# Optimization experiments

Measured on AMD Instinct MI355X. Metric: run time of the kernel, lower is better.

Reference implementation:

```python
import jax, jax.numpy as jnp
import numpy as np

EPS = 1e-5

def _layernorm(x, g, b):
    mu = jnp.mean(x, axis=-1, keepdims=True)
    var = jnp.mean(jnp.square(x - mu), axis=-1, keepdims=True)
    return (x - mu) * jax.lax.rsqrt(var + EPS) * g + b

def _knn_gather(x, idx):
    # x: (B, M, C), idx: (B, N, K) -> (B, N, K, C)
    return jax.vmap(lambda m, i: m[i])(x, idx)

def setup_inputs() -> dict:
    key = jax.random.key(0)
    B, N, M, K, C = 1, 8192, 8192, 32, 256
    ks = jax.random.split(key, 24)
    w = lambda k, *s: (jax.random.normal(k, s, dtype=jnp.float32) * 0.02)
    inp = {
        "input_states": jax.random.normal(ks[0], (B, N, C), dtype=jnp.float32),
        "memory_states": jax.random.normal(ks[1], (B, M, C), dtype=jnp.float32),
        "indices": jax.random.randint(ks[2], (B, N, K), 0, M, dtype=jnp.int32),
        "input_coord": jax.random.normal(ks[3], (B, N, 3), dtype=jnp.float32),
        "memory_coord": jax.random.normal(ks[4], (B, M, 3), dtype=jnp.float32),
        "attention_mask": jnp.ones((B, N, K), dtype=jnp.float32),
        "Wq": w(ks[5], C, C), "bq": jnp.zeros((C,), jnp.float32),
        "Wk": w(ks[6], C, C), "bk": jnp.zeros((C,), jnp.float32),
        "Wv": w(ks[7], C, C), "bv": jnp.zeros((C,), jnp.float32),
        "Wo": w(ks[8], C, C), "bo": jnp.zeros((C,), jnp.float32),
        "ln1_g": jnp.ones((C,), jnp.float32), "ln1_b": jnp.zeros((C,), jnp.float32),
        "Wrpe": w(ks[9], C // 2, 3), "brpe": jnp.zeros((C // 2,), jnp.float32),
        "We": w(ks[10], 2 * C, C), "be": jnp.zeros((2 * C,), jnp.float32),
        "Ws": w(ks[11], C, 2 * C), "bs": jnp.zeros((C,), jnp.float32),
        "ln2_g": jnp.ones((C,), jnp.float32), "ln2_b": jnp.zeros((C,), jnp.float32),
    }
    return inp

def reference(input_states, memory_states, indices, input_coord, memory_coord,
              attention_mask, Wq, bq, Wk, bk, Wv, bv, Wo, bo, ln1_g, ln1_b,
              Wrpe, brpe, We, be, Ws, bs, ln2_g, ln2_b):
    B, N, C = input_states.shape
    H = 8
    Ch = C // H
    q = input_states @ Wq.T + bq                                   # (B,N,C)
    k = _knn_gather(memory_states @ Wk.T + bk, indices)            # (B,N,K,C)
    v = _knn_gather(memory_states @ Wv.T + bv, indices)            # (B,N,K,C)
    # rotary positional encoding on relative coordinates
    rel = _knn_gather(memory_coord, indices) - input_coord[:, :, None, :]  # (B,N,K,3)
    ang = rel @ Wrpe.T + brpe                                      # (B,N,K,C/2)
    cos, sin = jnp.cos(ang), jnp.sin(ang)
    k2 = k.reshape(*k.shape[:-1], C // 2, 2)
    x0, x1 = k2[..., 0], k2[..., 1]
    k = jnp.stack([x0 * cos - x1 * sin, x0 * sin + x1 * cos], axis=-1).reshape(k.shape)
    # multi-head attention over K gathered neighbors
    qh = q.reshape(B, N, H, Ch)
    kh = k.reshape(B, N, -1, H, Ch)
    vh = v.reshape(B, N, -1, H, Ch)
    scores = jnp.einsum('bnhc,bnkhc->bhnk', qh, kh) / np.sqrt(Ch).astype(np.float32)
    scores = scores - 1e6 * (1.0 - attention_mask[:, None, :, :])
    attn = jax.nn.softmax(scores, axis=-1)
    hidden = jnp.einsum('bhnk,bnkhc->bnhc', attn, vh).reshape(B, N, C)
    hidden = hidden @ Wo.T + bo
    out = _layernorm(hidden + input_states, ln1_g, ln1_b)
    ff = jax.nn.relu(out @ We.T + be) @ Ws.T + bs
    return _layernorm(out + ff, ln2_g, ln2_b)
```

## Files before the change

kernel.cpp:

```cpp
#include <hip/hip_runtime.h>
#include <hip/hip_bf16.h>
#include <stdint.h>

typedef __attribute__((ext_vector_type(8))) __bf16 bf16x8;
typedef __attribute__((ext_vector_type(8))) unsigned short u16x8;
typedef __attribute__((ext_vector_type(4))) float f32x4;

__device__ inline float bf2f(unsigned short u) {
  union { unsigned u; float f; } z; z.u = ((unsigned)u) << 16; return z.f;
}
__device__ inline unsigned short f2bf(float f) {
  union { float f; unsigned u; } z; z.f = f;
  unsigned r = z.u + 0x7fffu + ((z.u >> 16) & 1u);
  return (unsigned short)(r >> 16);
}
__device__ inline void gload_lds16(const void* g, void* l) {
  __builtin_amdgcn_global_load_lds((const __attribute__((address_space(1))) void*)g,
                                   (__attribute__((address_space(3))) void*)l, 16, 0, 0);
}

__global__ __launch_bounds__(256, 2) void gemm_proj(
    const float* __restrict__ x, const float* __restrict__ mem,
    const float* __restrict__ Wq, const float* __restrict__ Wk, const float* __restrict__ Wv,
    const float* __restrict__ Wo, const float* __restrict__ We, const float* __restrict__ Ws,
    const float* __restrict__ Wrpe, const float* __restrict__ brpe,
    const float* __restrict__ bq, const float* __restrict__ bk, const float* __restrict__ bv,
    unsigned short* __restrict__ qbuf, unsigned short* __restrict__ kbp,
    unsigned short* __restrict__ vbp,
    unsigned short* __restrict__ wob, unsigned short* __restrict__ web,
    unsigned short* __restrict__ wsb, float4* __restrict__ rpe4) {
  const int tid = threadIdx.x;
  const int by = blockIdx.y;
  const long bm = blockIdx.x;

  if (by == 6) {
#pragma unroll
    for (int it = 0; it < 3; ++it) {
      const int j = (int)bm + 128 * it;
      if (j < 64) {
        const float4 v = *(const float4*)(Wo + (long)j * 1024 + tid * 4);
        ushort4 o; o.x = f2bf(v.x); o.y = f2bf(v.y); o.z = f2bf(v.z); o.w = f2bf(v.w);
        *(ushort4*)(wob + (long)j * 1024 + tid * 4) = o;
      } else if (j < 192) {
        const float4 v = *(const float4*)(We + (long)(j - 64) * 1024 + tid * 4);
        ushort4 o; o.x = f2bf(v.x); o.y = f2bf(v.y); o.z = f2bf(v.z); o.w = f2bf(v.w);
        *(ushort4*)(web + (long)(j - 64) * 1024 + tid * 4) = o;
      } else if (j < 320) {
        const float4 v = *(const float4*)(Ws + (long)(j - 192) * 1024 + tid * 4);
        ushort4 o; o.x = f2bf(v.x); o.y = f2bf(v.y); o.z = f2bf(v.z); o.w = f2bf(v.w);
        *(ushort4*)(wsb + (long)(j - 192) * 1024 + tid * 4) = o;
      } else if (j == 320) {
        if (tid < 128) {
          float4 r;
          r.x = Wrpe[3 * tid]; r.y = Wrpe[3 * tid + 1]; r.z = Wrpe[3 * tid + 2]; r.w = brpe[tid];
          rpe4[tid] = r;
        }
      }
    }
    return;
  }

  __shared__ __attribute__((aligned(16))) char lds[4096 + 8192];
  const int lane = tid & 63;
  const int wm = tid >> 7, wo = (tid >> 6) & 1;

  const float* Ab; const float* Wf; const float* biasp; unsigned short* outp; int cb;
  if (by < 2)      { Ab = x;   Wf = Wq + (long)by * 128 * 256;       biasp = bq + by * 128;       outp = qbuf; cb = by * 128; }
  else if (by < 4) { Ab = mem; Wf = Wk + (long)(by - 2) * 128 * 256; biasp = bk + (by - 2) * 128; outp = kbp;  cb = (by - 2) * 128; }
  else             { Ab = mem; Wf = Wv + (long)(by - 4) * 128 * 256; biasp = bv + (by - 4) * 128; outp = vbp;  cb = (by - 4) * 128; }

  f32x4 acc[2][4] = {};
  for (int kt = 0; kt < 8; ++kt) {
#pragma unroll
    for (int c = 0; c < 2; ++c) {
      const int fb = c * 4096 + tid * 16;
      const int row = fb >> 7, colb = fb & 127;
      const float4 a4 = *(const float4*)((const char*)Ab + (bm * 64 + row) * 1024 + kt * 128 + colb);
      ushort4 o; o.x = f2bf(a4.x); o.y = f2bf(a4.y); o.z = f2bf(a4.z); o.w = f2bf(a4.w);
      *(ushort4*)(lds + row * 64 + (colb >> 1)) = o;
    }
#pragma unroll
    for (int c = 0; c < 4; ++c) {
      const int fb = c * 4096 + tid * 16;
      const int row = fb >> 7, colb = fb & 127;
      const float4 a4 = *(const float4*)((const char*)Wf + (long)row * 1024 + kt * 128 + colb);
      ushort4 o; o.x = f2bf(a4.x); o.y = f2bf(a4.y); o.z = f2bf(a4.z); o.w = f2bf(a4.w);
      *(ushort4*)(lds + 4096 + row * 64 + (colb >> 1)) = o;
    }
    __syncthreads();
    bf16x8 af[2], bfr[4];
    const int kb = (lane >> 4) * 16;
#pragma unroll
    for (int i = 0; i < 2; ++i)
      af[i] = *(const bf16x8*)(lds + (wm * 32 + i * 16 + (lane & 15)) * 64 + kb);
#pragma unroll
    for (int j = 0; j < 4; ++j)
      bfr[j] = *(const bf16x8*)(lds + 4096 + (wo * 64 + j * 16 + (lane & 15)) * 64 + kb);
#pragma unroll
    for (int i = 0; i < 2; ++i)
#pragma unroll
      for (int j = 0; j < 4; ++j)
        acc[i][j] = __builtin_amdgcn_mfma_f32_16x16x32_bf16(af[i], bfr[j], acc[i][j], 0, 0, 0);
    __syncthreads();
  }

#pragma unroll
  for (int i = 0; i < 2; ++i) {
#pragma unroll
    for (int j = 0; j < 4; ++j) {
      const int lc = wo * 64 + j * 16 + (lane & 15);
      const float bvv = biasp[lc];
#pragma unroll
      for (int r = 0; r < 4; ++r) {
        const long rowg = bm * 64 + wm * 32 + i * 16 + (lane >> 4) * 4 + r;
        outp[rowg * 256 + cb + lc] = f2bf(acc[i][j][r] + bvv);
      }
    }
  }
}

__global__ __launch_bounds__(256, 4) void attn2(
    const unsigned short* __restrict__ qb,
    const unsigned short* __restrict__ kbp,
    const unsigned short* __restrict__ vbp,
    const int* __restrict__ idx,
    const float* __restrict__ icoord,
    const float* __restrict__ mcoord,
    const float* __restrict__ mask,
    const float4* __restrict__ rpe4,
    unsigned short* __restrict__ hb)
{
  __shared__ int idx_s[32];
  __shared__ float4 relm_s[32];
  __shared__ float4 rpe_s[128];
  __shared__ float p_s[256];
  __shared__ __attribute__((aligned(16))) unsigned short vls[32][256];

  const int n = blockIdx.x, t = threadIdx.x;
  if (t < 128) rpe_s[t] = rpe4[t];
  if (t < 32) {
    const int m = idx[n * 32 + t];
    idx_s[t] = m;
    float4 rm;
    rm.x = mcoord[(long)m * 3 + 0] - icoord[(long)n * 3 + 0];
    rm.y = mcoord[(long)m * 3 + 1] - icoord[(long)n * 3 + 1];
    rm.z = mcoord[(long)m * 3 + 2] - icoord[(long)n * 3 + 2];
    rm.w = mask[n * 32 + t];
    relm_s[t] = rm;
  }
  __syncthreads();

#pragma unroll
  for (int i = 0; i < 4; ++i) {
    const int b = i * 4096 + t * 16;
    const int r = b >> 9, cb = b & 511;
    gload_lds16((const char*)vbp + (long)idx_s[r] * 512 + cb, (char*)vls + b);
  }

  const int h = t >> 5, k = t & 31;
  const float4 rm = relm_s[k];
  const long krow = idx_s[k];

  u16x8 kv8[4], qv8[4];
  {
    const u16x8* kp = (const u16x8*)(kbp + krow * 256 + h * 32);
    const u16x8* qp = (const u16x8*)(qb + (long)n * 256 + h * 32);
#pragma unroll
    for (int i = 0; i < 4; ++i) { kv8[i] = kp[i]; qv8[i] = qp[i]; }
  }

  float sc = 0.f;
#pragma unroll
  for (int j2 = 0; j2 < 16; ++j2) {
    const float4 wj = rpe_s[h * 16 + j2];
    const float ang = fmaf(wj.x, rm.x, fmaf(wj.y, rm.y, fmaf(wj.z, rm.z, wj.w)));
    float sn, cs;
    __sincosf(ang, &sn, &cs);
    const int wi = j2 >> 2, e0 = (j2 & 3) * 2;
    const float x0 = bf2f(kv8[wi][e0]), x1 = bf2f(kv8[wi][e0 + 1]);
    const float q0 = bf2f(qv8[wi][e0]), q1 = bf2f(qv8[wi][e0 + 1]);
    const float k0 = fmaf(x0, cs, -x1 * sn);
    const float k1 = fmaf(x0, sn, x1 * cs);
    sc = fmaf(q0, k0, sc);
    sc = fmaf(q1, k1, sc);
  }
  sc = sc * 0.17677669529663687f - 1e6f * (1.f - rm.w);

  float mx = sc;
#pragma unroll
  for (int m = 16; m > 0; m >>= 1) mx = fmaxf(mx, __shfl_xor(mx, m, 32));
  const float e = __expf(sc - mx);
  float sum = e;
#pragma unroll
  for (int m = 16; m > 0; m >>= 1) sum += __shfl_xor(sum, m, 32);
  p_s[t] = e / sum;
  __syncthreads();

  float acc = 0.f;
#pragma unroll
  for (int k4 = 0; k4 < 8; ++k4) {
    const float4 p4 = *(const float4*)(p_s + (t >> 5) * 32 + k4 * 4);
    acc = fmaf(p4.x, bf2f(vls[k4 * 4 + 0][t]), acc);
    acc = fmaf(p4.y, bf2f(vls[k4 * 4 + 1][t]), acc);
    acc = fmaf(p4.z, bf2f(vls[k4 * 4 + 2][t]), acc);
    acc = fmaf(p4.w, bf2f(vls[k4 * 4 + 3][t]), acc);
  }
  hb[(long)n * 256 + t] = f2bf(acc);
}

__global__ __launch_bounds__(256) void megatail(
    const unsigned short* __restrict__ hb, const float* __restrict__ x,
    const unsigned short* __restrict__ wob, const unsigned short* __restrict__ web,
    const unsigned short* __restrict__ wsb,
    const float* __restrict__ bo, const float* __restrict__ g1, const float* __restrict__ b1,
    const float* __restrict__ be, const float* __restrict__ bs,
    const float* __restrict__ g2, const float* __restrict__ b2,
    float* __restrict__ outf) {
  __shared__ __attribute__((aligned(16))) char lds[65536];
  char* const out1_l = lds;
  char* const ffa_l  = lds + 16384;
  char* const wt_l   = lds + 49152;
  float2* const part = (float2*)(lds + 49152);

  const int tid = threadIdx.x, lane = tid & 63;
  const int wv = tid >> 6;
  const long bm = blockIdx.x;
  const int kb = (lane >> 4) * 16;
  const int lrow = (lane >> 4) * 4;
  const int c15 = lane & 15;
  int colg[4];
#pragma unroll
  for (int j = 0; j < 4; ++j) colg[j] = wv * 64 + j * 16 + c15;

  f32x4 acc[2][4];

#pragma unroll
  for (int p = 0; p < 4; ++p) {
    const int b = p * 4096 + tid * 16;
    gload_lds16((const char*)hb + (bm * 32 + (b >> 9)) * 512 + (b & 511), ffa_l + b);
  }
#pragma unroll
  for (int i = 0; i < 2; ++i)
#pragma unroll
    for (int j = 0; j < 4; ++j) acc[i][j] = (f32x4){0.f, 0.f, 0.f, 0.f};

  for (int kt = 0; kt < 8; ++kt) {
#pragma unroll
    for (int c = 0; c < 4; ++c) {
      const int b = c * 4096 + tid * 16;
      gload_lds16((const char*)wob + (long)(b >> 6) * 512 + kt * 64 + (b & 63), wt_l + b);
    }
    __syncthreads();
    bf16x8 af[2], bfq[4];
#pragma unroll
    for (int i = 0; i < 2; ++i)
      af[i] = *(const bf16x8*)(ffa_l + (i * 16 + c15) * 512 + kt * 64 + kb);
#pragma unroll
    for (int j = 0; j < 4; ++j)
      bfq[j] = *(const bf16x8*)(wt_l + (wv * 64 + j * 16 + c15) * 64 + kb);
#pragma unroll
    for (int i = 0; i < 2; ++i)
#pragma unroll
      for (int j = 0; j < 4; ++j)
        acc[i][j] = __builtin_amdgcn_mfma_f32_16x16x32_bf16(af[i], bfq[j], acc[i][j], 0, 0, 0);
    __syncthreads();
  }

#pragma unroll
  for (int i = 0; i < 2; ++i)
#pragma unroll
    for (int r = 0; r < 4; ++r) {
      const int rl = i * 16 + lrow + r;
      const long rowg = bm * 32 + rl;
#pragma unroll
      for (int j = 0; j < 4; ++j)
        acc[i][j][r] += bo[colg[j]] + x[rowg * 256 + colg[j]];
    }
#pragma unroll
  for (int i = 0; i < 2; ++i)
#pragma unroll
    for (int r = 0; r < 4; ++r) {
      const int rl = i * 16 + lrow + r;
      float s = 0.f, s2 = 0.f;
#pragma unroll
      for (int j = 0; j < 4; ++j) { const float v = acc[i][j][r]; s += v; s2 = fmaf(v, v, s2); }
#pragma unroll
      for (int m = 8; m > 0; m >>= 1) { s += __shfl_xor(s, m, 16); s2 += __shfl_xor(s2, m, 16); }
      if (c15 == 0) part[wv * 32 + rl] = make_float2(s, s2);
    }
  __syncthreads();
#pragma unroll
  for (int i = 0; i < 2; ++i)
#pragma unroll
    for (int r = 0; r < 4; ++r) {
      const int rl = i * 16 + lrow + r;
      float s = 0.f, s2 = 0.f;
#pragma unroll
      for (int q = 0; q < 4; ++q) { s += part[q * 32 + rl].x; s2 += part[q * 32 + rl].y; }
      const float mu = s * (1.f / 256.f);
      const float var = s2 * (1.f / 256.f) - mu * mu;
      const float inv = rsqrtf(var + 1e-5f);
#pragma unroll
      for (int j = 0; j < 4; ++j) {
        const float y = (acc[i][j][r] - mu) * inv * g1[colg[j]] + b1[colg[j]];
        *(unsigned short*)(out1_l + rl * 512 + colg[j] * 2) = f2bf(y);
      }
    }
  __syncthreads();

  for (int hc = 0; hc < 2; ++hc) {
#pragma unroll
    for (int i = 0; i < 2; ++i)
#pragma unroll
      for (int j = 0; j < 4; ++j) acc[i][j] = (f32x4){0.f, 0.f, 0.f, 0.f};
    for (int kt = 0; kt < 8; ++kt) {
#pragma unroll
      for (int c = 0; c < 4; ++c) {
        const int b = c * 4096 + tid * 16;
        gload_lds16((const char*)web + ((long)hc * 256 + (b >> 6)) * 512 + kt * 64 + (b & 63), wt_l + b);
      }
      __syncthreads();
      bf16x8 af[2], bfq[4];
#pragma unroll
      for (int i = 0; i < 2; ++i)
        af[i] = *(const bf16x8*)(out1_l + (i * 16 + c15) * 512 + kt * 64 + kb);
#pragma unroll
      for (int j = 0; j < 4; ++j)
        bfq[j] = *(const bf16x8*)(wt_l + (wv * 64 + j * 16 + c15) * 64 + kb);
#pragma unroll
      for (int i = 0; i < 2; ++i)
#pragma unroll
        for (int j = 0; j < 4; ++j)
          acc[i][j] = __builtin_amdgcn_mfma_f32_16x16x32_bf16(af[i], bfq[j], acc[i][j], 0, 0, 0);
      __syncthreads();
    }
#pragma unroll
    for (int i = 0; i < 2; ++i)
#pragma unroll
      for (int r = 0; r < 4; ++r) {
        const int rl = i * 16 + lrow + r;
#pragma unroll
        for (int j = 0; j < 4; ++j) {
          const int col = hc * 256 + colg[j];
          const float v = acc[i][j][r] + be[col];
          *(unsigned short*)(ffa_l + rl * 1024 + col * 2) = f2bf(v > 0.f ? v : 0.f);
        }
      }
  }

#pragma unroll
  for (int i = 0; i < 2; ++i)
#pragma unroll
    for (int j = 0; j < 4; ++j) acc[i][j] = (f32x4){0.f, 0.f, 0.f, 0.f};
  for (int kt = 0; kt < 16; ++kt) {
#pragma unroll
    for (int c = 0; c < 4; ++c) {
      const int b = c * 4096 + tid * 16;
      gload_lds16((const char*)wsb + (long)(b >> 6) * 1024 + kt * 64 + (b & 63), wt_l + b);
    }
    __syncthreads();
    bf16x8 af[2], bfq[4];
#pragma unroll
    for (int i = 0; i < 2; ++i)
      af[i] = *(const bf16x8*)(ffa_l + (i * 16 + c15) * 1024 + kt * 64 + kb);
#pragma unroll
    for (int j = 0; j < 4; ++j)
      bfq[j] = *(const bf16x8*)(wt_l + (wv * 64 + j * 16 + c15) * 64 + kb);
#pragma unroll
    for (int i = 0; i < 2; ++i)
#pragma unroll
      for (int j = 0; j < 4; ++j)
        acc[i][j] = __builtin_amdgcn_mfma_f32_16x16x32_bf16(af[i], bfq[j], acc[i][j], 0, 0, 0);
    __syncthreads();
  }
#pragma unroll
  for (int i = 0; i < 2; ++i)
#pragma unroll
    for (int r = 0; r < 4; ++r) {
      const int rl = i * 16 + lrow + r;
#pragma unroll
      for (int j = 0; j < 4; ++j)
        acc[i][j][r] += bs[colg[j]] + bf2f(*(const unsigned short*)(out1_l + rl * 512 + colg[j] * 2));
    }
#pragma unroll
  for (int i = 0; i < 2; ++i)
#pragma unroll
    for (int r = 0; r < 4; ++r) {
      const int rl = i * 16 + lrow + r;
      float s = 0.f, s2 = 0.f;
#pragma unroll
      for (int j = 0; j < 4; ++j) { const float v = acc[i][j][r]; s += v; s2 = fmaf(v, v, s2); }
#pragma unroll
      for (int m = 8; m > 0; m >>= 1) { s += __shfl_xor(s, m, 16); s2 += __shfl_xor(s2, m, 16); }
      if (c15 == 0) part[wv * 32 + rl] = make_float2(s, s2);
    }
  __syncthreads();
#pragma unroll
  for (int i = 0; i < 2; ++i)
#pragma unroll
    for (int r = 0; r < 4; ++r) {
      const int rl = i * 16 + lrow + r;
      const long rowg = bm * 32 + rl;
      float s = 0.f, s2 = 0.f;
#pragma unroll
      for (int q = 0; q < 4; ++q) { s += part[q * 32 + rl].x; s2 += part[q * 32 + rl].y; }
      const float mu = s * (1.f / 256.f);
      const float var = s2 * (1.f / 256.f) - mu * mu;
      const float inv = rsqrtf(var + 1e-5f);
#pragma unroll
      for (int j = 0; j < 4; ++j)
        outf[rowg * 256 + colg[j]] = (acc[i][j][r] - mu) * inv * g2[colg[j]] + b2[colg[j]];
    }
}

extern "C" void kernel_launch(void* const* d_in, const int* in_sizes, int n_in,
                              void* d_out, int out_size, void* d_ws, size_t ws_size,
                              hipStream_t stream) {
  const float* x    = (const float*)d_in[0];
  const float* mem  = (const float*)d_in[1];
  const int* idx    = (const int*)d_in[2];
  const float* ic   = (const float*)d_in[3];
  const float* mc   = (const float*)d_in[4];
  const float* mask = (const float*)d_in[5];
  const float* Wq = (const float*)d_in[6];  const float* bq = (const float*)d_in[7];
  const float* Wk = (const float*)d_in[8];  const float* bk = (const float*)d_in[9];
  const float* Wv = (const float*)d_in[10]; const float* bv = (const float*)d_in[11];
  const float* Wo = (const float*)d_in[12]; const float* bo = (const float*)d_in[13];
  const float* g1 = (const float*)d_in[14]; const float* b1 = (const float*)d_in[15];
  const float* Wrpe = (const float*)d_in[16]; const float* brpe = (const float*)d_in[17];
  const float* We = (const float*)d_in[18]; const float* be = (const float*)d_in[19];
  const float* Ws = (const float*)d_in[20]; const float* bs = (const float*)d_in[21];
  const float* g2 = (const float*)d_in[22]; const float* b2 = (const float*)d_in[23];

  char* w = (char*)d_ws;
  const size_t MB = 1ull << 20;
  unsigned short* kbp  = (unsigned short*)(w + 0);
  unsigned short* vbp  = (unsigned short*)(w + 4 * MB);
  unsigned short* qbuf = (unsigned short*)(w + 8 * MB);
  unsigned short* hb   = (unsigned short*)(w + 12 * MB);
  unsigned short* wob  = (unsigned short*)(w + 16 * MB);
  unsigned short* web  = wob + 65536;
  unsigned short* wsb  = web + 131072;
  float4*         rpe4 = (float4*)(wsb + 131072);

  gemm_proj<<<dim3(128, 7), 256, 0, stream>>>(
      x, mem, Wq, Wk, Wv, Wo, We, Ws, Wrpe, brpe, bq, bk, bv,
      qbuf, kbp, vbp, wob, web, wsb, rpe4);

  attn2<<<8192, 256, 0, stream>>>(qbuf, kbp, vbp, idx, ic, mc, mask, rpe4, hb);

  megatail<<<256, 256, 0, stream>>>(hb, x, wob, web, wsb,
                                    bo, g1, b1, be, bs, g2, b2, (float*)d_out);
}
```

Measured before the change: 84.72 us.

## Stage gathered K rows in LDS and halve megatail row tile with XOR swizzle

In the attention kernel, the gathered K rows are now loaded asynchronously into a swizzled LDS buffer alongside V, replacing the per-thread direct global loads. This coalesces the gather and overlaps it with the Q load, at the cost of extra LDS and a barrier. The tail kernel now processes 16 rows per block instead of 32, doubling the grid to 512 blocks with a smaller LDS footprint and two-blocks-per-CU launch bounds to raise occupancy. It also XOR-swizzles all LDS tiles to reduce bank conflicts, but each weight tile is now reloaded by twice as many blocks.

```diff
diff --git a/kernel.cpp b/kernel.cpp
--- a/kernel.cpp
+++ b/kernel.cpp
@@ -134,6 +134,7 @@
   __shared__ float4 relm_s[32];
   __shared__ float4 rpe_s[128];
   __shared__ float p_s[256];
+  __shared__ __attribute__((aligned(16))) unsigned short kls[32][256];
   __shared__ __attribute__((aligned(16))) unsigned short vls[32][256];
 
   const int n = blockIdx.x, t = threadIdx.x;
@@ -153,31 +154,35 @@
 #pragma unroll
   for (int i = 0; i < 4; ++i) {
     const int b = i * 4096 + t * 16;
-    const int r = b >> 9, cb = b & 511;
-    gload_lds16((const char*)vbp + (long)idx_s[r] * 512 + cb, (char*)vls + b);
+    const int r = b >> 9, c = b & 511;
+    gload_lds16((const char*)vbp + (long)idx_s[r] * 512 + c, (char*)vls + b);
+    gload_lds16((const char*)kbp + (long)idx_s[r] * 512 + (c ^ ((r & 7) << 4)), (char*)kls + b);
   }
 
   const int h = t >> 5, k = t & 31;
   const float4 rm = relm_s[k];
-  const long krow = idx_s[k];
-
-  u16x8 kv8[4], qv8[4];
+
+  u16x8 qv8[4];
   {
-    const u16x8* kp = (const u16x8*)(kbp + krow * 256 + h * 32);
     const u16x8* qp = (const u16x8*)(qb + (long)n * 256 + h * 32);
 #pragma unroll
-    for (int i = 0; i < 4; ++i) { kv8[i] = kp[i]; qv8[i] = qp[i]; }
-  }
+    for (int i = 0; i < 4; ++i) qv8[i] = qp[i];
+  }
+  __syncthreads();
 
   float sc = 0.f;
 #pragma unroll
   for (int j2 = 0; j2 < 16; ++j2) {
+    if ((j2 & 3) == 0) {
+    }
     const float4 wj = rpe_s[h * 16 + j2];
     const float ang = fmaf(wj.x, rm.x, fmaf(wj.y, rm.y, fmaf(wj.z, rm.z, wj.w)));
     float sn, cs;
     __sincosf(ang, &sn, &cs);
     const int wi = j2 >> 2, e0 = (j2 & 3) * 2;
-    const float x0 = bf2f(kv8[wi][e0]), x1 = bf2f(kv8[wi][e0 + 1]);
+    const bf16x8 kv = *(const bf16x8*)((const char*)kls + k * 512 + ((h * 64 + wi * 16) ^ ((k & 7) << 4)));
+    const u16x8 kvu = *(const u16x8*)&kv;
+    const float x0 = bf2f(kvu[e0]), x1 = bf2f(kvu[e0 + 1]);
     const float q0 = bf2f(qv8[wi][e0]), q1 = bf2f(qv8[wi][e0 + 1]);
     const float k0 = fmaf(x0, cs, -x1 * sn);
     const float k1 = fmaf(x0, sn, x1 * cs);
@@ -208,7 +213,7 @@
   hb[(long)n * 256 + t] = f2bf(acc);
 }
 
-__global__ __launch_bounds__(256) void megatail(
+__global__ __launch_bounds__(256, 2) void megatail2(
     const unsigned short* __restrict__ hb, const float* __restrict__ x,
     const unsigned short* __restrict__ wob, const unsigned short* __restrict__ web,
     const unsigned short* __restrict__ wsb,
@@ -216,201 +221,171 @@
     const float* __restrict__ be, const float* __restrict__ bs,
     const float* __restrict__ g2, const float* __restrict__ b2,
     float* __restrict__ outf) {
-  __shared__ __attribute__((aligned(16))) char lds[65536];
+  __shared__ __attribute__((aligned(16))) char lds[40960];
   char* const out1_l = lds;
-  char* const ffa_l  = lds + 16384;
-  char* const wt_l   = lds + 49152;
-  float2* const part = (float2*)(lds + 49152);
+  char* const ffa_l  = lds + 8192;
+  char* const wt_l   = lds + 24576;
+  float2* const part = (float2*)(lds + 24576);
 
   const int tid = threadIdx.x, lane = tid & 63;
-  const int wv = tid >> 6;
+  const int wv = tid >> 6, c15 = lane & 15;
+  const int kb = (lane >> 4) * 16, lrow = (lane >> 4) * 4;
   const long bm = blockIdx.x;
-  const int kb = (lane >> 4) * 16;
-  const int lrow = (lane >> 4) * 4;
-  const int c15 = lane & 15;
   int colg[4];
 #pragma unroll
   for (int j = 0; j < 4; ++j) colg[j] = wv * 64 + j * 16 + c15;
 
-  f32x4 acc[2][4];
-
-#pragma unroll
-  for (int p = 0; p < 4; ++p) {
+  f32x4 acc[4];
+
+#pragma unroll
+  for (int p = 0; p < 2; ++p) {
     const int b = p * 4096 + tid * 16;
-    gload_lds16((const char*)hb + (bm * 32 + (b >> 9)) * 512 + (b & 511), ffa_l + b);
-  }
-#pragma unroll
-  for (int i = 0; i < 2; ++i)
-#pragma unroll
-    for (int j = 0; j < 4; ++j) acc[i][j] = (f32x4){0.f, 0.f, 0.f, 0.f};
+    const int r = b >> 9, c = b & 511;
+    gload_lds16((const char*)hb + (bm * 16 + r) * 512 + (c ^ ((r & 7) << 4)), ffa_l + b);
+  }
+#pragma unroll
+  for (int j = 0; j < 4; ++j) acc[j] = (f32x4){0.f, 0.f, 0.f, 0.f};
 
   for (int kt = 0; kt < 8; ++kt) {
 #pragma unroll
     for (int c = 0; c < 4; ++c) {
       const int b = c * 4096 + tid * 16;
-      gload_lds16((const char*)wob + (long)(b >> 6) * 512 + kt * 64 + (b & 63), wt_l + b);
-    }
-    __syncthreads();
-    bf16x8 af[2], bfq[4];
-#pragma unroll
-    for (int i = 0; i < 2; ++i)
-      af[i] = *(const bf16x8*)(ffa_l + (i * 16 + c15) * 512 + kt * 64 + kb);
+      const int r = b >> 6, cc = b & 63;
+      gload_lds16((const char*)wob + (long)r * 512 + kt * 64 + (cc ^ (((r >> 2) & 3) << 4)), wt_l + b);
+    }
+    __syncthreads();
+    const bf16x8 af = *(const bf16x8*)(ffa_l + c15 * 512 + ((kt * 64 + kb) ^ ((c15 & 7) << 4)));
+    bf16x8 bq[4];
+#pragma unroll
+    for (int j = 0; j < 4; ++j) {
+      const int R = wv * 64 + j * 16 + c15;
+      bq[j] = *(const bf16x8*)(wt_l + R * 64 + (kb ^ (((R >> 2) & 3) << 4)));
+    }
 #pragma unroll
     for (int j = 0; j < 4; ++j)
-      bfq[j] = *(const bf16x8*)(wt_l + (wv * 64 + j * 16 + c15) * 64 + kb);
-#pragma unroll
-    for (int i = 0; i < 2; ++i)
-#pragma unroll
-      for (int j = 0; j < 4; ++j)
-        acc[i][j] = __builtin_amdgcn_mfma_f32_16x16x32_bf16(af[i], bfq[j], acc[i][j], 0, 0, 0);
-    __syncthreads();
-  }
-
-#pragma unroll
-  for (int i = 0; i < 2; ++i)
-#pragma unroll
-    for (int r = 0; r < 4; ++r) {
-      const int rl = i * 16 + lrow + r;
-      const long rowg = bm * 32 + rl;
-#pragma unroll
-      for (int j = 0; j < 4; ++j)
-        acc[i][j][r] += bo[colg[j]] + x[rowg * 256 + colg[j]];
-    }
-#pragma unroll
-  for (int i = 0; i < 2; ++i)
-#pragma unroll
-    for (int r = 0; r < 4; ++r) {
-      const int rl = i * 16 + lrow + r;
-      float s = 0.f, s2 = 0.f;
-#pragma unroll
-      for (int j = 0; j < 4; ++j) { const float v = acc[i][j][r]; s += v; s2 = fmaf(v, v, s2); }
-#pragma unroll
-      for (int m = 8; m > 0; m >>= 1) { s += __shfl_xor(s, m, 16); s2 += __shfl_xor(s2, m, 16); }
-      if (c15 == 0) part[wv * 32 + rl] = make_float2(s, s2);
-    }
-  __syncthreads();
-#pragma unroll
-  for (int i = 0; i < 2; ++i)
-#pragma unroll
-    for (int r = 0; r < 4; ++r) {
-      const int rl = i * 16 + lrow + r;
-      float s = 0.f, s2 = 0.f;
-#pragma unroll
-      for (int q = 0; q < 4; ++q) { s += part[q * 32 + rl].x; s2 += part[q * 32 + rl].y; }
-      const float mu = s * (1.f / 256.f);
-      const float var = s2 * (1.f / 256.f) - mu * mu;
-      const float inv = rsqrtf(var + 1e-5f);
-#pragma unroll
-      for (int j = 0; j < 4; ++j) {
-        const float y = (acc[i][j][r] - mu) * inv * g1[colg[j]] + b1[colg[j]];
-        *(unsigned short*)(out1_l + rl * 512 + colg[j] * 2) = f2bf(y);
-      }
-    }
+      acc[j] = __builtin_amdgcn_mfma_f32_16x16x32_bf16(af, bq[j], acc[j], 0, 0, 0);
+    __syncthreads();
+  }
+#pragma unroll
+  for (int r4 = 0; r4 < 4; ++r4) {
+    const int rl = lrow + r4;
+    const long rowg = bm * 16 + rl;
+    float s = 0.f, s2 = 0.f;
+#pragma unroll
+    for (int j = 0; j < 4; ++j) {
+      acc[j][r4] += bo[colg[j]] + x[rowg * 256 + colg[j]];
+      s += acc[j][r4]; s2 = fmaf(acc[j][r4], acc[j][r4], s2);
+    }
+#pragma unroll
+    for (int m = 8; m > 0; m >>= 1) { s += __shfl_xor(s, m, 16); s2 += __shfl_xor(s2, m, 16); }
+    if (c15 == 0) part[wv * 16 + rl] = make_float2(s, s2);
+  }
+  __syncthreads();
+#pragma unroll
+  for (int r4 = 0; r4 < 4; ++r4) {
+    const int rl = lrow + r4;
+    float s = 0.f, s2 = 0.f;
+#pragma unroll
+    for (int q = 0; q < 4; ++q) { s += part[q * 16 + rl].x; s2 += part[q * 16 + rl].y; }
+    const float mu = s * (1.f / 256.f);
+    const float var = s2 * (1.f / 256.f) - mu * mu;
+    const float inv = rsqrtf(var + 1e-5f);
+#pragma unroll
+    for (int j = 0; j < 4; ++j) {
+      const float y = (acc[j][r4] - mu) * inv * g1[colg[j]] + b1[colg[j]];
+      *(unsigned short*)(out1_l + rl * 512 + ((colg[j] * 2) ^ ((rl & 7) << 4))) = f2bf(y);
+    }
+  }
   __syncthreads();
 
   for (int hc = 0; hc < 2; ++hc) {
 #pragma unroll
-    for (int i = 0; i < 2; ++i)
-#pragma unroll
-      for (int j = 0; j < 4; ++j) acc[i][j] = (f32x4){0.f, 0.f, 0.f, 0.f};
+    for (int j = 0; j < 4; ++j) acc[j] = (f32x4){0.f, 0.f, 0.f, 0.f};
     for (int kt = 0; kt < 8; ++kt) {
 #pragma unroll
       for (int c = 0; c < 4; ++c) {
         const int b = c * 4096 + tid * 16;
-        gload_lds16((const char*)web + ((long)hc * 256 + (b >> 6)) * 512 + kt * 64 + (b & 63), wt_l + b);
+        const int r = b >> 6, cc = b & 63;
+        gload_lds16((const char*)web + ((long)hc * 256 + r) * 512 + kt * 64 + (cc ^ (((r >> 2) & 3) << 4)),
+                    wt_l + b);
       }
       __syncthreads();
-      bf16x8 af[2], bfq[4];
-#pragma unroll
-      for (int i = 0; i < 2; ++i)
-        af[i] = *(const bf16x8*)(out1_l + (i * 16 + c15) * 512 + kt * 64 + kb);
+      const bf16x8 af = *(const bf16x8*)(out1_l + c15 * 512 + ((kt * 64 + kb) ^ ((c15 & 7) << 4)));
+      bf16x8 bq[4];
+#pragma unroll
+      for (int j = 0; j < 4; ++j) {
+        const int R = wv * 64 + j * 16 + c15;
+        bq[j] = *(const bf16x8*)(wt_l + R * 64 + (kb ^ (((R >> 2) & 3) << 4)));
+      }
 #pragma unroll
       for (int j = 0; j < 4; ++j)
-        bfq[j] = *(const bf16x8*)(wt_l + (wv * 64 + j * 16 + c15) * 64 + kb);
-#pragma unroll
-      for (int i = 0; i < 2; ++i)
-#pragma unroll
-        for (int j = 0; j < 4; ++j)
-          acc[i][j] = __builtin_amdgcn_mfma_f32_16x16x32_bf16(af[i], bfq[j], acc[i][j], 0, 0, 0);
+        acc[j] = __builtin_amdgcn_mfma_f32_16x16x32_bf16(af, bq[j], acc[j], 0, 0, 0);
       __syncthreads();
     }
 #pragma unroll
-    for (int i = 0; i < 2; ++i)
-#pragma unroll
-      for (int r = 0; r < 4; ++r) {
-        const int rl = i * 16 + lrow + r;
-#pragma unroll
-        for (int j = 0; j < 4; ++j) {
-          const int col = hc * 256 + colg[j];
-          const float v = acc[i][j][r] + be[col];
-          *(unsigned short*)(ffa_l + rl * 1024 + col * 2) = f2bf(v > 0.f ? v : 0.f);
-        }
+    for (int r4 = 0; r4 < 4; ++r4) {
+      const int rl = lrow + r4;
+#pragma unroll
+      for (int j = 0; j < 4; ++j) {
+        const int col = hc * 256 + colg[j];
+        const float v = acc[j][r4] + be[col];
+        *(unsigned short*)(ffa_l + rl * 1024 + ((col * 2) ^ ((rl & 7) << 4))) = f2bf(v > 0.f ? v : 0.f);
       }
-  }
-
-#pragma unroll
-  for (int i = 0; i < 2; ++i)
-#pragma unroll
-    for (int j = 0; j < 4; ++j) acc[i][j] = (f32x4){0.f, 0.f, 0.f, 0.f};
+    }
+    __syncthreads();
+  }
+
+#pragma unroll
+  for (int j = 0; j < 4; ++j) acc[j] = (f32x4){0.f, 0.f, 0.f, 0.f};
   for (int kt = 0; kt < 16; ++kt) {
 #pragma unroll
     for (int c = 0; c < 4; ++c) {
       const int b = c * 4096 + tid * 16;
-      gload_lds16((const char*)wsb + (long)(b >> 6) * 1024 + kt * 64 + (b & 63), wt_l + b);
-    }
-    __syncthreads();
-    bf16x8 af[2], bfq[4];
-#pragma unroll
-    for (int i = 0; i < 2; ++i)
-      af[i] = *(const bf16x8*)(ffa_l + (i * 16 + c15) * 1024 + kt * 64 + kb);
+      const int r = b >> 6, cc = b & 63;
+      gload_lds16((const char*)wsb + (long)r * 1024 + kt * 64 + (cc ^ (((r >> 2) & 3) << 4)), wt_l + b);
+    }
+    __syncthreads();
+    const bf16x8 af = *(const bf16x8*)(ffa_l + c15 * 1024 + ((kt * 64 + kb) ^ ((c15 & 7) << 4)));
+    bf16x8 bq[4];
+#pragma unroll
+    for (int j = 0; j < 4; ++j) {
+      const int R = wv * 64 + j * 16 + c15;
+      bq[j] = *(const bf16x8*)(wt_l + R * 64 + (kb ^ (((R >> 2) & 3) << 4)));
+    }
 #pragma unroll
     for (int j = 0; j < 4; ++j)
-      bfq[j] = *(const bf16x8*)(wt_l + (wv * 64 + j * 16 + c15) * 64 + kb);
-#pragma unroll
-    for (int i = 0; i < 2; ++i)
-#pragma unroll
-      for (int j = 0; j < 4; ++j)
-        acc[i][j] = __builtin_amdgcn_mfma_f32_16x16x32_bf16(af[i], bfq[j], acc[i][j], 0, 0, 0);
-    __syncthreads();
-  }
-#pragma unroll
-  for (int i = 0; i < 2; ++i)
-#pragma unroll
-    for (int r = 0; r < 4; ++r) {
-      const int rl = i * 16 + lrow + r;
-#pragma unroll
-      for (int j = 0; j < 4; ++j)
-        acc[i][j][r] += bs[colg[j]] + bf2f(*(const unsigned short*)(out1_l + rl * 512 + colg[j] * 2));
-    }
-#pragma unroll
-  for (int i = 0; i < 2; ++i)
-#pragma unroll
-    for (int r = 0; r < 4; ++r) {
-      const int rl = i * 16 + lrow + r;
-      float s = 0.f, s2 = 0.f;
-#pragma unroll
-      for (int j = 0; j < 4; ++j) { const float v = acc[i][j][r]; s += v; s2 = fmaf(v, v, s2); }
-#pragma unroll
-      for (int m = 8; m > 0; m >>= 1) { s += __shfl_xor(s, m, 16); s2 += __shfl_xor(s2, m, 16); }
-      if (c15 == 0) part[wv * 32 + rl] = make_float2(s, s2);
-    }
-  __syncthreads();
-#pragma unroll
-  for (int i = 0; i < 2; ++i)
-#pragma unroll
-    for (int r = 0; r < 4; ++r) {
-      const int rl = i * 16 + lrow + r;
-      const long rowg = bm * 32 + rl;
-      float s = 0.f, s2 = 0.f;
-#pragma unroll
-      for (int q = 0; q < 4; ++q) { s += part[q * 32 + rl].x; s2 += part[q * 32 + rl].y; }
-      const float mu = s * (1.f / 256.f);
-      const float var = s2 * (1.f / 256.f) - mu * mu;
-      const float inv = rsqrtf(var + 1e-5f);
-#pragma unroll
-      for (int j = 0; j < 4; ++j)
-        outf[rowg * 256 + colg[j]] = (acc[i][j][r] - mu) * inv * g2[colg[j]] + b2[colg[j]];
-    }
+      acc[j] = __builtin_amdgcn_mfma_f32_16x16x32_bf16(af, bq[j], acc[j], 0, 0, 0);
+    __syncthreads();
+  }
+#pragma unroll
+  for (int r4 = 0; r4 < 4; ++r4) {
+    const int rl = lrow + r4;
+    float s = 0.f, s2 = 0.f;
+#pragma unroll
+    for (int j = 0; j < 4; ++j) {
+      const float res = bf2f(*(const unsigned short*)(out1_l + rl * 512 + ((colg[j] * 2) ^ ((rl & 7) << 4))));
+      acc[j][r4] += bs[colg[j]] + res;
+      s += acc[j][r4]; s2 = fmaf(acc[j][r4], acc[j][r4], s2);
+    }
+#pragma unroll
+    for (int m = 8; m > 0; m >>= 1) { s += __shfl_xor(s, m, 16); s2 += __shfl_xor(s2, m, 16); }
+    if (c15 == 0) part[wv * 16 + rl] = make_float2(s, s2);
+  }
+  __syncthreads();
+#pragma unroll
+  for (int r4 = 0; r4 < 4; ++r4) {
+    const int rl = lrow + r4;
+    const long rowg = bm * 16 + rl;
+    float s = 0.f, s2 = 0.f;
+#pragma unroll
+    for (int q = 0; q < 4; ++q) { s += part[q * 16 + rl].x; s2 += part[q * 16 + rl].y; }
+    const float mu = s * (1.f / 256.f);
+    const float var = s2 * (1.f / 256.f) - mu * mu;
+    const float inv = rsqrtf(var + 1e-5f);
+#pragma unroll
+    for (int j = 0; j < 4; ++j)
+      outf[rowg * 256 + colg[j]] = (acc[j][r4] - mu) * inv * g2[colg[j]] + b2[colg[j]];
+  }
 }
 
 extern "C" void kernel_launch(void* const* d_in, const int* in_sizes, int n_in,
@@ -449,6 +424,6 @@
 
   attn2<<<8192, 256, 0, stream>>>(qbuf, kbp, vbp, idx, ic, mc, mask, rpe4, hb);
 
-  megatail<<<256, 256, 0, stream>>>(hb, x, wob, web, wsb,
-                                    bo, g1, b1, be, bs, g2, b2, (float*)d_out);
-}
+  megatail2<<<512, 256, 0, stream>>>(hb, x, wob, web, wsb,
+                                     bo, g1, b1, be, bs, g2, b2, (float*)d_out);
+}
```

After: 86.67 us. +2.3%, slower.
